# Performance work log

Hardware: AMD Instinct MI355X
Metric: run time of the kernel (lower is better)

Reference implementation:

```python
import jax, jax.numpy as jnp
import numpy as np

DT = 0.01
REG = 0.01

def setup_inputs() -> dict:
    key = jax.random.key(0)
    k1, k2, k3, k4 = jax.random.split(key, 4)
    B, C_in, L = 16, 128, 4096
    C_out, KS = 256, 9
    return {
        "x": jax.random.normal(k1, (B, C_in, L), dtype=jnp.float32),
        "weight": jax.random.normal(k2, (C_out, C_in, KS), dtype=jnp.float32) * np.sqrt(2.0 / (C_out * KS)),
        "bias": jnp.zeros((C_out,), dtype=jnp.float32),
        "vel": jax.random.normal(k3, (C_in, KS), dtype=jnp.float32) * 0.1,
        "acc": jax.random.normal(k4, (C_in, KS), dtype=jnp.float32) * 0.01,
        "ks": 9,
        "stride": 1,
        "pad": 4,
    }

def reference(x, weight, bias, vel, acc, ks, stride, pad):
    # x: [B, C_in, L]
    if pad > 0:
        x = jnp.pad(x, ((0, 0), (0, 0), (pad, pad)), mode="edge")  # replicate pad
    L_pad = x.shape[2]
    L_out = (L_pad - ks) // stride + 1
    t_off = jnp.arange(ks, dtype=jnp.float32) * DT  # [ks]
    # unfold: gather sliding windows -> [B, C_in, L_out, ks]
    idx = jnp.arange(L_out)[:, None] * stride + jnp.arange(ks)[None, :]
    xu = x[:, :, idx]
    # per-tap physics offset: vel*t + 0.5*acc*t^2, shape [C_in, ks] broadcast
    offset = vel * t_off + 0.5 * acc * (t_off ** 2)  # [C_in, ks]
    xt = xu + offset[None, :, None, :]  # [B, C_in, L_out, ks]
    # GEMM: [B, L_out, C_in*ks] x [C_in*ks, C_out]
    out = jnp.einsum("bclk,ock->bol", xt, weight) + bias[None, :, None]
    phys = REG * (jnp.mean(vel ** 2) + jnp.mean(acc ** 2))
    return (out, phys)
```

## Files before the change

kernel.cpp:

```cpp
#include <hip/hip_runtime.h>
#include <hip/hip_bf16.h>

typedef unsigned short u16;
typedef __bf16 bf16x8 __attribute__((ext_vector_type(8)));
typedef float f32x4 __attribute__((ext_vector_type(4)));
typedef float f32x16 __attribute__((ext_vector_type(16)));
typedef unsigned short ushort8 __attribute__((ext_vector_type(8)));

#define C_IN   128
#define C_OUT  256
#define BATCH  16
#define LEN    4096
#define KS     9
#define PAD    4
#define LPAD   (LEN + 2*PAD)
#define KTOT   (C_IN * KS)
#define NSTEP  72

#define XT_BLKS    1040
#define W5_BLKS    1152
#define EB_BLKS    256

__device__ inline u16 f2bf(float f) {
    __hip_bfloat16 h = __float2bfloat16(f);
    return __builtin_bit_cast(u16, h);
}

__device__ __forceinline__ void g2l16(const void* g, void* l) {
    __builtin_amdgcn_global_load_lds(
        (const __attribute__((address_space(1))) void*)g,
        (__attribute__((address_space(3))) void*)l, 16, 0, 0);
}

__global__ void prep_all(const float* __restrict__ x, const float* __restrict__ w,
                         const float* __restrict__ bias, const float* __restrict__ vel,
                         const float* __restrict__ acc_in,
                         u16* __restrict__ xt, u16* __restrict__ w5,
                         float* __restrict__ ebias, float* __restrict__ phys_out) {
    int bid = blockIdx.x;
    int t = threadIdx.x;
    if (bid < XT_BLKS) {
        int b    = bid / 65;
        int lblk = bid % 65;
        int lane = t & 63;
        int jb   = t >> 6;
        int lp   = lblk * 64 + lane;
        if (lp >= LPAD) return;
        int l = lp - PAD;
        l = l < 0 ? 0 : (l > LEN - 1 ? LEN - 1 : l);
        const float* xb = x + (size_t)b * C_IN * LEN + l;
        u16* row = xt + ((size_t)b * LPAD + lp) * C_IN;
        int key = lp & 15;
        #pragma unroll
        for (int jj = 0; jj < 4; ++jj) {
            int cblk = jb * 4 + jj;
            ushort8 v;
            #pragma unroll
            for (int e = 0; e < 8; ++e)
                v[e] = f2bf(xb[(size_t)(cblk * 8 + e) * LEN]);
            int jstore = cblk ^ key;
            *reinterpret_cast<ushort8*>(row + jstore * 8) = v;
        }
        return;
    }
    if (bid < XT_BLKS + W5_BLKS) {
        int i = (bid - XT_BLKS) * 256 + t;
        int e    = i & 7;
        int lane = (i >> 3) & 63;
        int g    = (i >> 9) & 7;
        int s    = i >> 12;
        int o    = g * 32 + (lane & 31);
        int hi   = lane >> 5;
        int c    = (s & 7) * 16 + hi * 8 + e;
        int k    = s >> 3;
        w5[i] = f2bf(w[((size_t)o * C_IN + c) * KS + k]);
        return;
    }
    __shared__ float red[256];
    int o = bid - (XT_BLKS + W5_BLKS);
    float sum = 0.f;
    for (int i = t; i < KTOT; i += 256) {
        int k = i % KS;
        float tk = k * 0.01f;
        float off = vel[i] * tk + 0.5f * acc_in[i] * tk * tk;
        sum += off * w[(size_t)o * KTOT + i];
    }
    red[t] = sum;
    __syncthreads();
    for (int h = 128; h > 0; h >>= 1) {
        if (t < h) red[t] += red[t + h];
        __syncthreads();
    }
    if (t == 0) ebias[o] = bias[o] + red[0];

    if (o == 0) {
        __syncthreads();
        float pv = 0.f;
        for (int i = t; i < KTOT; i += 256) {
            float v = vel[i], a = acc_in[i];
            pv += v * v + a * a;
        }
        red[t] = pv;
        __syncthreads();
        for (int h = 128; h > 0; h >>= 1) {
            if (t < h) red[t] += red[t + h];
            __syncthreads();
        }
        if (t == 0) *phys_out = 0.01f * (red[0] / (float)KTOT);
    }
}

__global__ __launch_bounds__(128, 1) void conv_main(const u16* __restrict__ xt,
                                                    const u16* __restrict__ w5,
                                                    const float* __restrict__ ebias,
                                                    float* __restrict__ out) {
    __shared__ u16 ldsx[17408];

    int b     = blockIdx.y;
    int lbase = blockIdx.x * 128;
    int t     = threadIdx.x;
    int lane  = t & 63;
    int wm    = t >> 6;
    int l31   = lane & 31;
    int hi    = lane >> 5;

    const u16* alane = w5 + ((size_t)(wm * 4) * 64 + lane) * 8;

    #define LOAD_A(S, AF)                                                        \
        {                                                                        \
            const u16* p_ = alane + (size_t)(S) * 4096;                          \
            _Pragma("unroll")                                                    \
            for (int mi = 0; mi < 4; ++mi)                                       \
                AF[mi] = *reinterpret_cast<const bf16x8*>(p_ + mi * 512);        \
        }
    #define LOAD_B(S, BF)                                                        \
        {                                                                        \
            int k_ = (S) >> 3;                                                   \
            int sl_ = ((S) & 7) * 2 + hi;                                        \
            _Pragma("unroll")                                                    \
            for (int nj = 0; nj < 4; ++nj) {                                     \
                int row_  = nj * 32 + l31 + k_;                                  \
                int addr_ = row_ * 256 + ((sl_ ^ (row_ & 15)) << 4);             \
                BF[nj] = *reinterpret_cast<const bf16x8*>(ldsbase + addr_);      \
            }                                                                    \
        }
    #define MFMA16(AF, BF)                                                       \
        {                                                                        \
            _Pragma("unroll")                                                    \
            for (int mi = 0; mi < 4; ++mi)                                       \
                _Pragma("unroll")                                                \
                for (int nj = 0; nj < 4; ++nj)                                   \
                    acc[mi][nj] = __builtin_amdgcn_mfma_f32_32x32x16_bf16(       \
                        AF[mi], BF[nj], acc[mi][nj], 0, 0, 0);                   \
        }

    bf16x8 aA[4], aB[4], bA[4], bB[4];

    {
        const u16* bsrc = xt + ((size_t)b * LPAD + lbase) * C_IN;
        #pragma unroll
        for (int j = 0; j < 17; ++j)
            g2l16(bsrc + (j * 128 + t) * 8, ldsx + (j * 128 + wm * 64) * 8);
    }
    LOAD_A(0, aA);
    __syncthreads();

    f32x16 acc[4][4] = {};
    const char* ldsbase = reinterpret_cast<const char*>(ldsx);
    LOAD_B(0, bA);

    #pragma unroll
    for (int s = 0; s < NSTEP; s += 2) {
        LOAD_A(s + 1, aB);
        LOAD_B(s + 1, bB);
        MFMA16(aA, bA);
        if (s + 2 < NSTEP) { LOAD_A(s + 2, aA); LOAD_B(s + 2, bA); }
        MFMA16(aB, bB);
    }

    #pragma unroll
    for (int mi = 0; mi < 4; ++mi) {
        int o0 = wm * 128 + mi * 32 + hi * 4;
        #pragma unroll
        for (int nj = 0; nj < 4; ++nj) {
            int l = lbase + nj * 32 + l31;
            #pragma unroll
            for (int q = 0; q < 4; ++q) {
                f32x4 eb = *reinterpret_cast<const f32x4*>(ebias + o0 + q * 8);
                float* op = out + (size_t)(b * C_OUT + o0 + q * 8) * LEN + l;
                #pragma unroll
                for (int p = 0; p < 4; ++p)
                    op[(size_t)p * LEN] = acc[mi][nj][q * 4 + p] + eb[p];
            }
        }
    }
    #undef LOAD_A
    #undef LOAD_B
    #undef MFMA16
}

extern "C" void kernel_launch(void* const* d_in, const int* in_sizes, int n_in,
                              void* d_out, int out_size, void* d_ws, size_t ws_size,
                              hipStream_t stream) {
    const float* x      = (const float*)d_in[0];
    const float* weight = (const float*)d_in[1];
    const float* bias   = (const float*)d_in[2];
    const float* vel    = (const float*)d_in[3];
    const float* acc    = (const float*)d_in[4];
    float* out = (float*)d_out;

    char* ws = (char*)d_ws;
    u16*  xt    = (u16*)ws;
    u16*  w5    = (u16*)(ws + (size_t)BATCH * LPAD * C_IN * 2);
    float* ebias = (float*)(ws + (size_t)BATCH * LPAD * C_IN * 2 + (size_t)C_OUT * KTOT * 2);

    hipLaunchKernelGGL(prep_all, dim3(XT_BLKS + W5_BLKS + EB_BLKS), dim3(256), 0, stream,
                       x, weight, bias, vel, acc, xt, w5, ebias,
                       out + (size_t)BATCH * C_OUT * LEN);
    hipLaunchKernelGGL(conv_main, dim3(LEN / 128, BATCH), dim3(128), 0, stream,
                       xt, w5, ebias, out);
}
```

Baseline: 57.64 us.

## Stream weight fragments through an LDS ring via async global-to-LDS loads

Weight (A) fragments were loaded straight from global memory into registers one step ahead. They now go through a per-wave 4-slot LDS ring, filled three steps ahead with global_load_lds and gated by explicit vmcnt waits, then read from LDS. This is meant to hide global-memory latency on the weight stream behind the MFMA work. In exchange it adds 32KB of LDS and extra LDS read traffic, and it relies on hand-counted vmcnt values with no barrier, since each wave only reads the ring slots it filled itself.

```diff
diff --git a/kernel.cpp b/kernel.cpp
--- a/kernel.cpp
+++ b/kernel.cpp
@@ -115,6 +115,7 @@
                                                     const float* __restrict__ ebias,
                                                     float* __restrict__ out) {
     __shared__ u16 ldsx[17408];
+    __shared__ u16 ldsa[2 * 4 * 2048];
 
     int b     = blockIdx.y;
     int lbase = blockIdx.x * 128;
@@ -125,13 +126,22 @@
     int hi    = lane >> 5;
 
     const u16* alane = w5 + ((size_t)(wm * 4) * 64 + lane) * 8;
-
-    #define LOAD_A(S, AF)                                                        \
+    u16* aring = ldsa + wm * 8192;
+
+    #define STAGE_A(S)                                                           \
         {                                                                        \
             const u16* p_ = alane + (size_t)(S) * 4096;                          \
+            u16* d_ = aring + ((S) & 3) * 2048;                                  \
             _Pragma("unroll")                                                    \
             for (int mi = 0; mi < 4; ++mi)                                       \
-                AF[mi] = *reinterpret_cast<const bf16x8*>(p_ + mi * 512);        \
+                g2l16(p_ + mi * 512, d_ + mi * 512);                             \
+        }
+    #define LOAD_A(BUF, AF)                                                      \
+        {                                                                        \
+            const u16* ab_ = aring + (BUF) * 2048 + lane * 8;                    \
+            _Pragma("unroll")                                                    \
+            for (int mi = 0; mi < 4; ++mi)                                       \
+                AF[mi] = *reinterpret_cast<const bf16x8*>(ab_ + mi * 512);       \
         }
     #define LOAD_B(S, BF)                                                        \
         {                                                                        \
@@ -153,6 +163,15 @@
                     acc[mi][nj] = __builtin_amdgcn_mfma_f32_32x32x16_bf16(       \
                         AF[mi], BF[nj], acc[mi][nj], 0, 0, 0);                   \
         }
+    #define WAITV(S)                                                             \
+        {                                                                        \
+            if ((S) + 3 < NSTEP)                                                 \
+                asm volatile("s_waitcnt vmcnt(8)" ::: "memory");                 \
+            else if ((S) + 2 < NSTEP)                                            \
+                asm volatile("s_waitcnt vmcnt(4)" ::: "memory");                 \
+            else if ((S) + 1 < NSTEP)                                            \
+                asm volatile("s_waitcnt vmcnt(0)" ::: "memory");                 \
+        }
 
     bf16x8 aA[4], aB[4], bA[4], bB[4];
 
@@ -161,20 +180,28 @@
         #pragma unroll
         for (int j = 0; j < 17; ++j)
             g2l16(bsrc + (j * 128 + t) * 8, ldsx + (j * 128 + wm * 64) * 8);
-    }
-    LOAD_A(0, aA);
+        STAGE_A(0); STAGE_A(1); STAGE_A(2);
+    }
     __syncthreads();
 
     f32x16 acc[4][4] = {};
     const char* ldsbase = reinterpret_cast<const char*>(ldsx);
+    LOAD_A(0, aA);
     LOAD_B(0, bA);
 
     #pragma unroll
     for (int s = 0; s < NSTEP; s += 2) {
-        LOAD_A(s + 1, aB);
+        if (s + 3 < NSTEP) STAGE_A(s + 3);
+        WAITV(s);
+        LOAD_A((s + 1) & 3, aB);
         LOAD_B(s + 1, bB);
         MFMA16(aA, bA);
-        if (s + 2 < NSTEP) { LOAD_A(s + 2, aA); LOAD_B(s + 2, bA); }
+        if (s + 4 < NSTEP) STAGE_A(s + 4);
+        if (s + 2 < NSTEP) {
+            WAITV(s + 1);
+            LOAD_A((s + 2) & 3, aA);
+            LOAD_B(s + 2, bA);
+        }
         MFMA16(aB, bB);
     }
 
@@ -194,9 +221,11 @@
             }
         }
     }
+    #undef STAGE_A
     #undef LOAD_A
     #undef LOAD_B
     #undef MFMA16
+    #undef WAITV
 }
 
 extern "C" void kernel_launch(void* const* d_in, const int* in_sizes, int n_in,
```

After: 60.25 us. +4.5%, slower.

## Fuse input transpose and bf16 conversion into conv kernel, drop xt staging buffer

Applied to the files above, without the earlier changes.

Removes the prep stage that wrote a padded, transposed bf16 copy of x to global memory. The conv kernel now reads fp32 x directly, applies edge clamping, converts to bf16 and writes the swizzled tile into LDS itself. This saves a full global write and reread of the activation tensor. The cost is that each block now issues many strided scalar fp32 loads before its MFMA loop, and those loads are not overlapped with compute.

```diff
diff --git a/kernel.cpp b/kernel.cpp
--- a/kernel.cpp
+++ b/kernel.cpp
@@ -13,11 +13,9 @@
 #define LEN    4096
 #define KS     9
 #define PAD    4
-#define LPAD   (LEN + 2*PAD)
 #define KTOT   (C_IN * KS)
 #define NSTEP  72
 
-#define XT_BLKS    1040
 #define W5_BLKS    1152
 #define EB_BLKS    256
 
@@ -32,39 +30,15 @@
         (__attribute__((address_space(3))) void*)l, 16, 0, 0);
 }
 
-__global__ void prep_all(const float* __restrict__ x, const float* __restrict__ w,
+__global__ void prep_all(const float* __restrict__ w,
                          const float* __restrict__ bias, const float* __restrict__ vel,
                          const float* __restrict__ acc_in,
-                         u16* __restrict__ xt, u16* __restrict__ w5,
+                         u16* __restrict__ w5,
                          float* __restrict__ ebias, float* __restrict__ phys_out) {
     int bid = blockIdx.x;
     int t = threadIdx.x;
-    if (bid < XT_BLKS) {
-        int b    = bid / 65;
-        int lblk = bid % 65;
-        int lane = t & 63;
-        int jb   = t >> 6;
-        int lp   = lblk * 64 + lane;
-        if (lp >= LPAD) return;
-        int l = lp - PAD;
-        l = l < 0 ? 0 : (l > LEN - 1 ? LEN - 1 : l);
-        const float* xb = x + (size_t)b * C_IN * LEN + l;
-        u16* row = xt + ((size_t)b * LPAD + lp) * C_IN;
-        int key = lp & 15;
-        #pragma unroll
-        for (int jj = 0; jj < 4; ++jj) {
-            int cblk = jb * 4 + jj;
-            ushort8 v;
-            #pragma unroll
-            for (int e = 0; e < 8; ++e)
-                v[e] = f2bf(xb[(size_t)(cblk * 8 + e) * LEN]);
-            int jstore = cblk ^ key;
-            *reinterpret_cast<ushort8*>(row + jstore * 8) = v;
-        }
-        return;
-    }
-    if (bid < XT_BLKS + W5_BLKS) {
-        int i = (bid - XT_BLKS) * 256 + t;
+    if (bid < W5_BLKS) {
+        int i = bid * 256 + t;
         int e    = i & 7;
         int lane = (i >> 3) & 63;
         int g    = (i >> 9) & 7;
@@ -77,7 +51,7 @@
         return;
     }
     __shared__ float red[256];
-    int o = bid - (XT_BLKS + W5_BLKS);
+    int o = bid - W5_BLKS;
     float sum = 0.f;
     for (int i = t; i < KTOT; i += 256) {
         int k = i % KS;
@@ -110,7 +84,7 @@
     }
 }
 
-__global__ __launch_bounds__(128, 1) void conv_main(const u16* __restrict__ xt,
+__global__ __launch_bounds__(128, 1) void conv_main(const float* __restrict__ x,
                                                     const u16* __restrict__ w5,
                                                     const float* __restrict__ ebias,
                                                     float* __restrict__ out) {
@@ -155,14 +129,39 @@
         }
 
     bf16x8 aA[4], aB[4], bA[4], bB[4];
-
+    LOAD_A(0, aA);
+
+    const float* xb = x + (size_t)b * C_IN * LEN;
     {
-        const u16* bsrc = xt + ((size_t)b * LPAD + lbase) * C_IN;
-        #pragma unroll
-        for (int j = 0; j < 17; ++j)
-            g2l16(bsrc + (j * 128 + t) * 8, ldsx + (j * 128 + wm * 64) * 8);
-    }
-    LOAD_A(0, aA);
+        int r = t;
+        int l = lbase + r - PAD;
+        l = l < 0 ? 0 : (l > LEN - 1 ? LEN - 1 : l);
+        int key = r & 15;
+        float v[16][8];
+        #pragma unroll
+        for (int cb = 0; cb < 16; ++cb)
+            #pragma unroll
+            for (int e = 0; e < 8; ++e)
+                v[cb][e] = xb[(size_t)(cb * 8 + e) * LEN + l];
+        #pragma unroll
+        for (int cb = 0; cb < 16; ++cb) {
+            ushort8 u;
+            #pragma unroll
+            for (int e = 0; e < 8; ++e) u[e] = f2bf(v[cb][e]);
+            *reinterpret_cast<ushort8*>(ldsx + r * 128 + ((cb ^ key) * 8)) = u;
+        }
+    }
+    {
+        int r  = 128 + (t & 7);
+        int cb = t >> 3;
+        int l = lbase + r - PAD;
+        l = l < 0 ? 0 : (l > LEN - 1 ? LEN - 1 : l);
+        ushort8 u;
+        #pragma unroll
+        for (int e = 0; e < 8; ++e)
+            u[e] = f2bf(xb[(size_t)(cb * 8 + e) * LEN + l]);
+        *reinterpret_cast<ushort8*>(ldsx + r * 128 + ((cb ^ (r & 15)) * 8)) = u;
+    }
     __syncthreads();
 
     f32x16 acc[4][4] = {};
@@ -210,13 +209,12 @@
     float* out = (float*)d_out;
 
     char* ws = (char*)d_ws;
-    u16*  xt    = (u16*)ws;
-    u16*  w5    = (u16*)(ws + (size_t)BATCH * LPAD * C_IN * 2);
-    float* ebias = (float*)(ws + (size_t)BATCH * LPAD * C_IN * 2 + (size_t)C_OUT * KTOT * 2);
-
-    hipLaunchKernelGGL(prep_all, dim3(XT_BLKS + W5_BLKS + EB_BLKS), dim3(256), 0, stream,
-                       x, weight, bias, vel, acc, xt, w5, ebias,
+    u16*  w5    = (u16*)ws;
+    float* ebias = (float*)(ws + (size_t)C_OUT * KTOT * 2);
+
+    hipLaunchKernelGGL(prep_all, dim3(W5_BLKS + EB_BLKS), dim3(256), 0, stream,
+                       weight, bias, vel, acc, w5, ebias,
                        out + (size_t)BATCH * C_OUT * LEN);
     hipLaunchKernelGGL(conv_main, dim3(LEN / 128, BATCH), dim3(128), 0, stream,
-                       xt, w5, ebias, out);
-}
+                       x, w5, ebias, out);
+}
```

New measurement: 51.79 us. -10.1%, faster.
